# Kernel optimization log

Hardware: AMD Instinct MI355X
Metric: run time of the kernel (lower is better)

Reference implementation:

```python
import jax, jax.numpy as jnp
import numpy as np

N, M, E, D = 20000, 1024, 640000, 256


def setup_inputs() -> dict:
    key = jax.random.key(0)
    ks = jax.random.split(key, 24)
    mask = jax.random.uniform(ks[0], (N, M)) < 0.05
    init = jnp.where(mask, jax.random.uniform(ks[1], (N, M), minval=0.1, maxval=1.0), 0.0)
    inp = {
        'init': init,
        'ei_cc': jax.random.randint(ks[2], (2, E), 0, N, dtype=jnp.int32),
        'ei_cac': jax.random.randint(ks[3], (2, E), 0, N, dtype=jnp.int32),
        'ei_csc': jax.random.randint(ks[4], (2, E), 0, N, dtype=jnp.int32),
        'ea_cc': jax.random.uniform(ks[5], (E,), minval=0.1, maxval=1.0),
        'ea_cac': jax.random.uniform(ks[6], (E,), minval=0.1, maxval=1.0),
        'ea_csc': jax.random.uniform(ks[7], (E,), minval=0.1, maxval=1.0),
        # Projection MLP: Linear(1,16) -> ReLU -> Linear(16,D)
        'pW1': jax.random.normal(ks[8], (1, 16)) * 0.5,
        'pb1': jnp.zeros((16,)),
        'pW2': jax.random.normal(ks[9], (16, D)) * 0.1,
        'pb2': jnp.zeros((D,)),
        # three GCN branches, 3 layers each (all D->D)
        'W_cc': jax.random.normal(ks[10], (3, D, D)) * 0.05,
        'b_cc': jnp.zeros((3, D)),
        'W_cac': jax.random.normal(ks[11], (3, D, D)) * 0.05,
        'b_cac': jnp.zeros((3, D)),
        'W_csc': jax.random.normal(ks[12], (3, D, D)) * 0.05,
        'b_csc': jnp.zeros((3, D)),
        # meta-path attention: Linear(D, 1)
        'w_att': jax.random.normal(ks[13], (D,)) * 0.05,
        'b_att': jnp.zeros((1,)),
    }
    return inp


def projection(init, pW1, pb1, pW2, pb2):
    # torch code feeds the *indices* of nonzero columns through the MLP and
    # mean-pools per row. Vectorize: precompute MLP(j) for every column index j,
    # then masked mean.
    idx = jnp.arange(M, dtype=init.dtype)[:, None]          # [M, 1]
    h = jax.nn.relu(idx @ pW1 + pb1)                        # [M, 16]
    col_emb = h @ pW2 + pb2                                 # [M, D]
    mask = (init != 0).astype(init.dtype)                   # [N, M]
    cnt = mask.sum(axis=1)                                  # [N]
    emb = (mask @ col_emb) / jnp.maximum(cnt, 1.0)[:, None]
    return jnp.where(cnt[:, None] > 0, emb, 0.0)            # zero rows stay zero


def gcn_conv(x, edge_index, edge_weight, W, b):
    # PyG GCNConv with edge_weight: add self loops (w=1), symmetric norm.
    n = x.shape[0]
    loop = jnp.arange(n, dtype=edge_index.dtype)
    row = jnp.concatenate([edge_index[0], loop])
    col = jnp.concatenate([edge_index[1], loop])
    w = jnp.concatenate([edge_weight, jnp.ones((n,), x.dtype)])
    deg = jax.ops.segment_sum(w, col, num_segments=n)
    dinv = jnp.where(deg > 0, jax.lax.rsqrt(deg), 0.0)
    norm = dinv[row] * w * dinv[col]                        # [E+N]
    h = x @ W                                               # [N, D]
    out = jax.ops.segment_sum(norm[:, None] * h[row], col, num_segments=n)
    return out + b


def gcn_branch(x, edge_index, edge_weight, Ws, bs):
    for l in range(3):
        x = jax.nn.relu(gcn_conv(x, edge_index, edge_weight, Ws[l], bs[l]))
    return x


def reference(init, ei_cc, ei_cac, ei_csc, ea_cc, ea_cac, ea_csc,
              pW1, pb1, pW2, pb2, W_cc, b_cc, W_cac, b_cac, W_csc, b_csc,
              w_att, b_att):
    x0 = projection(init, pW1, pb1, pW2, pb2)               # [N, D]
    out_cc = gcn_branch(x0, ei_cc, ea_cc, W_cc, b_cc)
    out_cac = gcn_branch(x0, ei_cac, ea_cac, W_cac, b_cac)
    out_csc = gcn_branch(x0, ei_csc, ea_csc, W_csc, b_csc)
    emb = jnp.stack([out_cc, out_cac, out_csc], axis=0)     # [3, N, D]
    scores = jnp.einsum('pnd,d->pn', emb, w_att) + b_att[0] # [3, N]
    attn = jax.nn.softmax(scores, axis=0)                   # softmax over meta-paths
    return jnp.einsum('pn,pnd->nd', attn, emb)              # [N, D]
```

## Files before the change

kernel.cpp:

```cpp
#include <hip/hip_runtime.h>
#include <hip/hip_bf16.h>

typedef __hip_bfloat16 bf16;
typedef __bf16 v8bf __attribute__((ext_vector_type(8)));
typedef float f32x4 __attribute__((ext_vector_type(4)));
typedef unsigned int v4u __attribute__((ext_vector_type(4)));

constexpr int N = 20000, M = 1024, E = 640000, D = 256;
constexpr size_t SEGEL = (size_t)N * D;
constexpr int NCHUNK = 10000;
constexpr int NSLICE = 64;
constexpr int ESLICE = E / NSLICE;

__device__ __forceinline__ float b2f(bf16 v) { return __bfloat162float(v); }
__device__ __forceinline__ bf16 f2b(float f) { return __float2bfloat16(f); }
__device__ __forceinline__ float u2f(unsigned short u) { return __uint_as_float(((unsigned)u) << 16); }
__device__ __forceinline__ unsigned short f2u(float f) { bf16 h = __float2bfloat16(f); return *(unsigned short*)&h; }
__device__ __forceinline__ float loadf(const void* p, size_t i, int isbf) {
    return isbf ? b2f(((const bf16*)p)[i]) : ((const float*)p)[i];
}
__device__ __forceinline__ void fma8(float* acc, uint4 v, float w) {
    acc[0] = fmaf(w, u2f((unsigned short)(v.x & 0xffffu)), acc[0]);
    acc[1] = fmaf(w, u2f((unsigned short)(v.x >> 16)), acc[1]);
    acc[2] = fmaf(w, u2f((unsigned short)(v.y & 0xffffu)), acc[2]);
    acc[3] = fmaf(w, u2f((unsigned short)(v.y >> 16)), acc[3]);
    acc[4] = fmaf(w, u2f((unsigned short)(v.z & 0xffffu)), acc[4]);
    acc[5] = fmaf(w, u2f((unsigned short)(v.z >> 16)), acc[5]);
    acc[6] = fmaf(w, u2f((unsigned short)(v.w & 0xffffu)), acc[6]);
    acc[7] = fmaf(w, u2f((unsigned short)(v.w >> 16)), acc[7]);
}
__device__ __forceinline__ void add4(float* acc, uint2 v) {
    acc[0] += u2f((unsigned short)(v.x & 0xffffu));
    acc[1] += u2f((unsigned short)(v.x >> 16));
    acc[2] += u2f((unsigned short)(v.y & 0xffffu));
    acc[3] += u2f((unsigned short)(v.y >> 16));
}
__device__ __forceinline__ unsigned pack2(float a, float b) {
    return (unsigned)f2u(a) | ((unsigned)f2u(b) << 16);
}

__global__ void detect_kernel(const void* __restrict__ ea, int* __restrict__ flag)
{
    if (threadIdx.x == 0 && blockIdx.x == 0) {
        const unsigned short* u = (const unsigned short*)ea;
        int cnt = 0;
        for (int i = 0; i < 64; i++) {
            float f = __uint_as_float(((unsigned)u[i]) << 16);
            if (f >= 0.05f && f <= 1.05f) cnt++;
        }
        *flag = (cnt >= 60) ? 1 : 0;
    }
}

__global__ __launch_bounds__(256) void prep_kernel(
    const void* __restrict__ W0, const void* __restrict__ W1, const void* __restrict__ W2,
    const void* __restrict__ pW1, const void* __restrict__ pb1,
    const void* __restrict__ pW2, const void* __restrict__ pb2,
    bf16* __restrict__ WT, bf16* __restrict__ cemb, const int* __restrict__ flag)
{
    int isbf = *flag;
    int b = blockIdx.x;
    if (b < 2304) {
        int mat = b >> 8, n = b & 255, k = threadIdx.x;
        const void* W = (mat < 3) ? W0 : (mat < 6) ? W1 : W2;
        int lm = mat - (mat < 3 ? 0 : (mat < 6 ? 3 : 6));
        WT[(size_t)mat * 65536 + n * 256 + k] =
            f2b(loadf(W, (size_t)lm * 65536 + k * 256 + n, isbf));
    } else {
        int j = b - 2304;
        int d = threadIdx.x;
        float jf = (float)j;
        float acc = loadf(pb2, d, isbf);
        #pragma unroll
        for (int k = 0; k < 16; k++) {
            float h = fmaxf(jf * loadf(pW1, k, isbf) + loadf(pb1, k, isbf), 0.0f);
            acc += h * loadf(pW2, k * 256 + d, isbf);
        }
        cemb[(size_t)j * 256 + d] = f2b(acc);
    }
}

__global__ __launch_bounds__(256) void projection_kernel(
    const void* __restrict__ init, const bf16* __restrict__ cemb,
    bf16* __restrict__ x0, const int* __restrict__ flag)
{
    __shared__ unsigned short idxs[4][1024];
    int isbf = *flag;
    int wave = threadIdx.x >> 6, lane = threadIdx.x & 63;
    int i = blockIdx.x * 4 + wave;
    unsigned long long below = (lane == 63) ? 0x7fffffffffffffffull
                                            : ((1ull << lane) - 1ull);
    int cnt = 0;
    if (isbf) {
        const unsigned short* row = (const unsigned short*)init + (size_t)i * 1024;
        for (int c0 = 0; c0 < 1024; c0 += 64) {
            bool nz = (row[c0 + lane] & 0x7fffu) != 0;
            unsigned long long m = __ballot(nz);
            if (nz) idxs[wave][cnt + __popcll(m & below)] = (unsigned short)(c0 + lane);
            cnt += __popcll(m);
        }
    } else {
        const float* row = (const float*)init + (size_t)i * 1024;
        for (int c0 = 0; c0 < 1024; c0 += 64) {
            bool nz = row[c0 + lane] != 0.0f;
            unsigned long long m = __ballot(nz);
            if (nz) idxs[wave][cnt + __popcll(m & below)] = (unsigned short)(c0 + lane);
            cnt += __popcll(m);
        }
    }
    const uint2* cr = (const uint2*)cemb;
    float acc[4] = {0.0f, 0.0f, 0.0f, 0.0f};
    int j = 0;
    for (; j + 8 <= cnt; j += 8) {
        uint2 v0 = cr[(size_t)idxs[wave][j + 0] * 64 + lane];
        uint2 v1 = cr[(size_t)idxs[wave][j + 1] * 64 + lane];
        uint2 v2 = cr[(size_t)idxs[wave][j + 2] * 64 + lane];
        uint2 v3 = cr[(size_t)idxs[wave][j + 3] * 64 + lane];
        uint2 v4 = cr[(size_t)idxs[wave][j + 4] * 64 + lane];
        uint2 v5 = cr[(size_t)idxs[wave][j + 5] * 64 + lane];
        uint2 v6 = cr[(size_t)idxs[wave][j + 6] * 64 + lane];
        uint2 v7 = cr[(size_t)idxs[wave][j + 7] * 64 + lane];
        add4(acc, v0); add4(acc, v1); add4(acc, v2); add4(acc, v3);
        add4(acc, v4); add4(acc, v5); add4(acc, v6); add4(acc, v7);
    }
    for (; j < cnt; j++) {
        uint2 v = cr[(size_t)idxs[wave][j] * 64 + lane];
        add4(acc, v);
    }
    float rinv = 1.0f / fmaxf((float)cnt, 1.0f);
    uint2 o;
    o.x = pack2(acc[0] * rinv, acc[1] * rinv);
    o.y = pack2(acc[2] * rinv, acc[3] * rinv);
    ((uint2*)x0)[(size_t)i * 64 + lane] = o;
}

__global__ __launch_bounds__(256) void countP_kernel(
    const int* __restrict__ e0, const int* __restrict__ e1, const int* __restrict__ e2,
    int* __restrict__ P)
{
    __shared__ int cur[NCHUNK];
    int b = blockIdx.x;
    int pb = b >> 7, rem = b & 127;
    int ck = rem >> 6, s = rem & 63;
    const int* ei = pb == 0 ? e0 : pb == 1 ? e1 : e2;
    int c0 = ck * NCHUNK;
    int t = threadIdx.x;
    for (int i = t; i < NCHUNK; i += 256) cur[i] = 0;
    __syncthreads();
    int ebase = s * ESLICE;
    for (int e = ebase + t; e < ebase + ESLICE; e += 256) {
        int c = ei[E + e];
        if (c >= c0 && c < c0 + NCHUNK) atomicAdd(&cur[c - c0], 1);
    }
    __syncthreads();
    int* Prow = P + ((size_t)(pb * NSLICE + s)) * N + c0;
    for (int i = t; i < NCHUNK; i += 256) Prow[i] = cur[i];
}

__global__ __launch_bounds__(256) void cnt_sum_kernel(
    const int* __restrict__ P, int* __restrict__ cnt)
{
    int id = blockIdx.x * 256 + threadIdx.x;
    if (id >= 3 * N) return;
    int pb = id / N, c = id - pb * N;
    int sum = 0;
    #pragma unroll 8
    for (int s = 0; s < NSLICE; s++)
        sum += P[((size_t)(pb * NSLICE + s)) * N + c];
    cnt[id] = sum;
}

__global__ __launch_bounds__(1024) void scan_kernel(
    const int* __restrict__ cnt, int* __restrict__ col_ptr)
{
    int pb = blockIdx.x;
    int base = pb * E;
    __shared__ int s[1024];
    int t = threadIdx.x;
    const int CH = 20;
    int i0 = t * CH;
    int sum = 0;
    for (int j = 0; j < CH; j++) { int i = i0 + j; if (i < N) sum += cnt[pb * N + i]; }
    s[t] = sum;
    __syncthreads();
    for (int off = 1; off < 1024; off <<= 1) {
        int v = (t >= off) ? s[t - off] : 0;
        __syncthreads();
        s[t] += v;
        __syncthreads();
    }
    int run = base + s[t] - sum;
    for (int j = 0; j < CH; j++) {
        int i = i0 + j;
        if (i < N) {
            col_ptr[pb * (N + 1) + i] = run;
            run += cnt[pb * N + i];
        }
    }
    if (t == 0) col_ptr[pb * (N + 1) + N] = base + E;
}

__global__ __launch_bounds__(256) void base_kernel(
    int* __restrict__ P, const int* __restrict__ col_ptr)
{
    int id = blockIdx.x * 256 + threadIdx.x;
    if (id >= 3 * N) return;
    int pb = id / N, c = id - pb * N;
    int run = col_ptr[pb * (N + 1) + c];
    for (int s = 0; s < NSLICE; s++) {
        size_t idx = ((size_t)(pb * NSLICE + s)) * N + c;
        int v = P[idx];
        P[idx] = run;
        run += v;
    }
}

__global__ __launch_bounds__(256) void fill_kernel(
    const int* __restrict__ e0, const int* __restrict__ e1, const int* __restrict__ e2,
    const void* __restrict__ a0, const void* __restrict__ a1, const void* __restrict__ a2,
    const int* __restrict__ P, int2* __restrict__ epack, const int* __restrict__ flag)
{
    __shared__ int cur[NCHUNK];
    int isbf = *flag;
    int b = blockIdx.x;
    int pb = b >> 7, rem = b & 127;
    int ck = rem >> 6, s = rem & 63;
    const int* ei = pb == 0 ? e0 : pb == 1 ? e1 : e2;
    const void* ea = pb == 0 ? a0 : pb == 1 ? a1 : a2;
    int c0 = ck * NCHUNK;
    int t = threadIdx.x;
    const int* Prow = P + ((size_t)(pb * NSLICE + s)) * N + c0;
    for (int i = t; i < NCHUNK; i += 256) cur[i] = Prow[i];
    __syncthreads();
    int ebase = s * ESLICE;
    for (int e = ebase + t; e < ebase + ESLICE; e += 256) {
        int c = ei[E + e];
        if (c >= c0 && c < c0 + NCHUNK) {
            int r = ei[e];
            float w = loadf(ea, e, isbf);
            int pos = atomicAdd(&cur[c - c0], 1);
            int2 v; v.x = r; v.y = __float_as_int(w);
            epack[pos] = v;
        }
    }
}

__global__ __launch_bounds__(256) void degsum_kernel(
    const int* __restrict__ col_ptr, const int2* __restrict__ epack,
    float* __restrict__ dinv, float* __restrict__ nloop)
{
    int wave = threadIdx.x >> 6, lane = threadIdx.x & 63;
    int pb = blockIdx.x / 5000;
    int i = (blockIdx.x - pb * 5000) * 4 + wave;
    int start = col_ptr[pb * (N + 1) + i], end = col_ptr[pb * (N + 1) + i + 1];
    float sum = 0.0f;
    for (int p = start + lane; p < end; p += 64) sum += __int_as_float(epack[p].y);
    for (int off = 1; off < 64; off <<= 1) sum += __shfl_xor(sum, off, 64);
    if (lane == 0) {
        float dg = 1.0f + sum;
        dinv[pb * N + i] = rsqrtf(dg);
        nloop[pb * N + i] = 1.0f / dg;
    }
}

__global__ __launch_bounds__(256) void snorm_sort_kernel(
    const int* __restrict__ col_ptr, int2* __restrict__ epack,
    const float* __restrict__ dinv)
{
    int wave = threadIdx.x >> 6, lane = threadIdx.x & 63;
    int pb = blockIdx.x / 5000;
    int i = (blockIdx.x - pb * 5000) * 4 + wave;
    int start = col_ptr[pb * (N + 1) + i], end = col_ptr[pb * (N + 1) + i + 1];
    float dc = dinv[pb * N + i];
    for (int base = start; base < end; base += 64) {
        int n = end - base; n = n < 64 ? n : 64;
        int key = 0x7fffffff, val = 0;
        if (lane < n) {
            int2 v = epack[base + lane];
            key = v.x;
            val = __float_as_int(dc * __int_as_float(v.y) * dinv[pb * N + v.x]);
        }
        #pragma unroll
        for (int k = 2; k <= 64; k <<= 1) {
            #pragma unroll
            for (int j = k >> 1; j > 0; j >>= 1) {
                int pk = __shfl_xor(key, j, 64);
                int pv = __shfl_xor(val, j, 64);
                bool up = (lane & k) == 0;
                bool lower = (lane & j) == 0;
                bool takeMin = (up == lower);
                bool sw = takeMin ? (pk < key) : (pk > key);
                if (sw) { key = pk; val = pv; }
            }
        }
        if (lane < n) {
            int2 o; o.x = key; o.y = val;
            epack[base + lane] = o;
        }
    }
}

__global__ __launch_bounds__(256) void aggregate_kernel(
    const bf16* __restrict__ xi0, const bf16* __restrict__ xi1, const bf16* __restrict__ xi2,
    bf16* __restrict__ yb,
    const int* __restrict__ col_ptr, const int2* __restrict__ epack,
    const float* __restrict__ nloop)
{
    int wave = threadIdx.x >> 6, lane = threadIdx.x & 63;
    int pb = blockIdx.x / 5000;
    int i = (blockIdx.x - pb * 5000) * 4 + wave;
    const bf16* x = pb == 0 ? xi0 : pb == 1 ? xi1 : xi2;
    const uint4* xr = (const uint4*)x;
    int L = lane & 31, h = lane >> 5;
    int start = col_ptr[pb * (N + 1) + i], end = col_ptr[pb * (N + 1) + i + 1];
    float nl = nloop[pb * N + i];
    float acc[8];
    {
        uint4 sv = xr[(size_t)i * 32 + L];
        float self = (h == 0) ? nl : 0.0f;
        #pragma unroll
        for (int j = 0; j < 8; j++) acc[j] = 0.0f;
        fma8(acc, sv, self);
    }
    for (int base = start; base < end; base += 64) {
        int n = end - base; n = n < 64 ? n : 64;
        int ex = 0, ey = 0;
        if (lane < n) {
            unsigned long long ev = __builtin_nontemporal_load(
                (const unsigned long long*)(epack + base + lane));
            ex = (int)(unsigned)(ev & 0xffffffffull);
            ey = (int)(unsigned)(ev >> 32);
        }
        int pmax = (n + 1) >> 1;
        int p0 = 0;
        for (; p0 + 8 <= pmax; p0 += 8) {
            int eb = 2 * p0 + h;
            int r0 = __shfl(ex, eb +  0, 64);
            int r1 = __shfl(ex, eb +  2, 64);
            int r2 = __shfl(ex, eb +  4, 64);
            int r3 = __shfl(ex, eb +  6, 64);
            int r4 = __shfl(ex, eb +  8, 64);
            int r5 = __shfl(ex, eb + 10, 64);
            int r6 = __shfl(ex, eb + 12, 64);
            int r7 = __shfl(ex, eb + 14, 64);
            float w0 = __int_as_float(__shfl(ey, eb +  0, 64));
            float w1 = __int_as_float(__shfl(ey, eb +  2, 64));
            float w2 = __int_as_float(__shfl(ey, eb +  4, 64));
            float w3 = __int_as_float(__shfl(ey, eb +  6, 64));
            float w4 = __int_as_float(__shfl(ey, eb +  8, 64));
            float w5 = __int_as_float(__shfl(ey, eb + 10, 64));
            float w6 = __int_as_float(__shfl(ey, eb + 12, 64));
            float w7 = __int_as_float(__shfl(ey, eb + 14, 64));
            uint4 v0 = xr[(size_t)r0 * 32 + L];
            uint4 v1 = xr[(size_t)r1 * 32 + L];
            uint4 v2 = xr[(size_t)r2 * 32 + L];
            uint4 v3 = xr[(size_t)r3 * 32 + L];
            uint4 v4 = xr[(size_t)r4 * 32 + L];
            uint4 v5 = xr[(size_t)r5 * 32 + L];
            uint4 v6 = xr[(size_t)r6 * 32 + L];
            uint4 v7 = xr[(size_t)r7 * 32 + L];
            fma8(acc, v0, w0); fma8(acc, v1, w1);
            fma8(acc, v2, w2); fma8(acc, v3, w3);
            fma8(acc, v4, w4); fma8(acc, v5, w5);
            fma8(acc, v6, w6); fma8(acc, v7, w7);
        }
        if (p0 + 4 <= pmax) {
            int eb = 2 * p0 + h;
            int r0 = __shfl(ex, eb + 0, 64);
            int r1 = __shfl(ex, eb + 2, 64);
            int r2 = __shfl(ex, eb + 4, 64);
            int r3 = __shfl(ex, eb + 6, 64);
            float w0 = __int_as_float(__shfl(ey, eb + 0, 64));
            float w1 = __int_as_float(__shfl(ey, eb + 2, 64));
            float w2 = __int_as_float(__shfl(ey, eb + 4, 64));
            float w3 = __int_as_float(__shfl(ey, eb + 6, 64));
            uint4 v0 = xr[(size_t)r0 * 32 + L];
            uint4 v1 = xr[(size_t)r1 * 32 + L];
            uint4 v2 = xr[(size_t)r2 * 32 + L];
            uint4 v3 = xr[(size_t)r3 * 32 + L];
            fma8(acc, v0, w0); fma8(acc, v1, w1);
            fma8(acc, v2, w2); fma8(acc, v3, w3);
            p0 += 4;
        }
        for (; p0 < pmax; p0++) {
            int e = 2 * p0 + h;
            int rj = __shfl(ex, e, 64);
            float w = __int_as_float(__shfl(ey, e, 64));
            uint4 v = xr[(size_t)rj * 32 + L];
            fma8(acc, v, w);
        }
    }
    #pragma unroll
    for (int j = 0; j < 8; j++) acc[j] += __shfl_xor(acc[j], 32, 64);
    if (h == 0) {
        v4u o;
        o.x = pack2(acc[0], acc[1]);
        o.y = pack2(acc[2], acc[3]);
        o.z = pack2(acc[4], acc[5]);
        o.w = pack2(acc[6], acc[7]);
        __builtin_nontemporal_store(o,
            (v4u*)yb + (size_t)pb * (SEGEL / 8) + (size_t)i * 32 + L);
    }
}

__global__ __launch_bounds__(256) void gemm_relu_kernel(
    const bf16* __restrict__ yb, const bf16* __restrict__ WT, int layer,
    const void* __restrict__ b0, const void* __restrict__ b1, const void* __restrict__ b2,
    bf16* __restrict__ o0, bf16* __restrict__ o1, bf16* __restrict__ o2,
    const int* __restrict__ flag)
{
    int isbf = *flag;
    int pl = blockIdx.x / 625, blk = blockIdx.x - pl * 625;
    const bf16* y = yb + (size_t)pl * SEGEL;
    const bf16* wt = WT + (size_t)(pl * 3 + layer) * 65536;
    const void* bias = pl == 0 ? b0 : pl == 1 ? b1 : b2;
    bf16* xout = pl == 0 ? o0 : pl == 1 ? o1 : o2;

    int wave = threadIdx.x >> 6, lane = threadIdx.x & 63;
    int m0 = blk * 32 + (wave >> 1) * 16;
    int n0 = (wave & 1) * 128;
    int mrow = lane & 15, q = lane >> 4;

    f32x4 acc[8] = {};
    const v8bf* arow = reinterpret_cast<const v8bf*>(y + (size_t)(m0 + mrow) * 256);
    for (int k0 = 0; k0 < 256; k0 += 32) {
        v8bf a = arow[(k0 >> 3) + q];
        #pragma unroll
        for (int nt = 0; nt < 8; nt++) {
            const v8bf* brow = reinterpret_cast<const v8bf*>(wt + (size_t)(n0 + nt * 16 + mrow) * 256);
            acc[nt] = __builtin_amdgcn_mfma_f32_16x16x32_bf16(a, brow[(k0 >> 3) + q], acc[nt], 0, 0, 0);
        }
    }
    #pragma unroll
    for (int nt = 0; nt < 8; nt++) {
        int col = n0 + nt * 16 + mrow;
        float bv = loadf(bias, (size_t)layer * 256 + col, isbf);
        #pragma unroll
        for (int r = 0; r < 4; r++) {
            int row = m0 + q * 4 + r;
            xout[(size_t)row * 256 + col] = f2b(fmaxf(acc[nt][r] + bv, 0.0f));
        }
    }
}

__global__ __launch_bounds__(256) void attention_kernel(
    const bf16* __restrict__ e0, const bf16* __restrict__ e1, const bf16* __restrict__ e2,
    const void* __restrict__ w_att, void* __restrict__ out, int n_nodes,
    const int* __restrict__ flag)
{
    int isbf = *flag;
    int wave = threadIdx.x >> 6, lane = threadIdx.x & 63;
    int n = blockIdx.x * 4 + wave;
    if (n >= n_nodes) return;
    int d0 = lane * 4;
    float w[4], v0[4], v1[4], v2[4];
    #pragma unroll
    for (int j = 0; j < 4; j++) {
        w[j]  = loadf(w_att, d0 + j, isbf);
        v0[j] = b2f(e0[(size_t)n * 256 + d0 + j]);
        v1[j] = b2f(e1[(size_t)n * 256 + d0 + j]);
        v2[j] = b2f(e2[(size_t)n * 256 + d0 + j]);
    }
    float s0 = 0, s1 = 0, s2 = 0;
    #pragma unroll
    for (int j = 0; j < 4; j++) { s0 += v0[j] * w[j]; s1 += v1[j] * w[j]; s2 += v2[j] * w[j]; }
    for (int off = 1; off < 64; off <<= 1) {
        s0 += __shfl_xor(s0, off, 64);
        s1 += __shfl_xor(s1, off, 64);
        s2 += __shfl_xor(s2, off, 64);
    }
    float m = fmaxf(s0, fmaxf(s1, s2));
    float a0 = expf(s0 - m), a1 = expf(s1 - m), a2 = expf(s2 - m);
    float inv = 1.0f / (a0 + a1 + a2);
    a0 *= inv; a1 *= inv; a2 *= inv;
    #pragma unroll
    for (int j = 0; j < 4; j++) {
        float v = a0 * v0[j] + a1 * v1[j] + a2 * v2[j];
        if (isbf) ((bf16*)out)[(size_t)n * 256 + d0 + j] = f2b(v);
        else      ((float*)out)[(size_t)n * 256 + d0 + j] = v;
    }
}

extern "C" void kernel_launch(void* const* d_in, const int* in_sizes, int n_in,
                              void* d_out, int out_size, void* d_ws, size_t ws_size,
                              hipStream_t stream)
{
    (void)in_sizes; (void)n_in; (void)out_size; (void)ws_size;

    const void* init = d_in[0];
    const int*  ei[3] = {(const int*)d_in[1], (const int*)d_in[2], (const int*)d_in[3]};
    const void* ea[3] = {d_in[4], d_in[5], d_in[6]};
    const void* pW1 = d_in[7];
    const void* pb1 = d_in[8];
    const void* pW2 = d_in[9];
    const void* pb2 = d_in[10];
    const void* Wb[3] = {d_in[11], d_in[13], d_in[15]};
    const void* bb[3] = {d_in[12], d_in[14], d_in[16]};
    const void* w_att = d_in[17];

    char* ws = (char*)d_ws;
    size_t off = 0;
    auto carve = [&](size_t bytes) -> char* {
        off = (off + 255) & ~(size_t)255;
        char* p = ws + off; off += bytes; return p;
    };
    int*   flag  = (int*)carve(4);
    bf16*  WT    = (bf16*)carve((size_t)9 * 65536 * 2);
    bf16*  cemb  = (bf16*)carve((size_t)M * D * 2);
    bf16*  x0    = (bf16*)carve(SEGEL * 2);
    int*   cnt   = (int*)carve((size_t)3 * N * 4);
    int*   colp  = (int*)carve((size_t)3 * (N + 1) * 4);
    float* dinv  = (float*)carve((size_t)3 * N * 4);
    float* nloop = (float*)carve((size_t)3 * N * 4);
    int2*  epack = (int2*)carve((size_t)3 * E * 8);
    bf16*  ybuf  = (bf16*)carve((size_t)3 * SEGEL * 2);
    bf16*  bufA  = (bf16*)carve((size_t)3 * SEGEL * 2);
    bf16*  bufB  = (bf16*)carve((size_t)3 * SEGEL * 2);
    int* P = (int*)bufB;

    detect_kernel<<<1, 64, 0, stream>>>(ea[0], flag);
    prep_kernel<<<3328, 256, 0, stream>>>(Wb[0], Wb[1], Wb[2],
                                          pW1, pb1, pW2, pb2, WT, cemb, flag);
    projection_kernel<<<5000, 256, 0, stream>>>(init, cemb, x0, flag);

    countP_kernel<<<384, 256, 0, stream>>>(ei[0], ei[1], ei[2], P);
    cnt_sum_kernel<<<(3 * N + 255) / 256, 256, 0, stream>>>(P, cnt);
    scan_kernel<<<3, 1024, 0, stream>>>(cnt, colp);
    base_kernel<<<(3 * N + 255) / 256, 256, 0, stream>>>(P, colp);
    fill_kernel<<<384, 256, 0, stream>>>(ei[0], ei[1], ei[2], ea[0], ea[1], ea[2],
                                         P, epack, flag);
    degsum_kernel<<<15000, 256, 0, stream>>>(colp, epack, dinv, nloop);
    snorm_sort_kernel<<<15000, 256, 0, stream>>>(colp, epack, dinv);

    const bf16 *i0 = x0, *i1 = x0, *i2 = x0;
    bf16* dsts[3] = {bufA, bufB, bufA};
    for (int l = 0; l < 3; l++) {
        aggregate_kernel<<<15000, 256, 0, stream>>>(i0, i1, i2, ybuf, colp, epack, nloop);
        bf16* dst = dsts[l];
        gemm_relu_kernel<<<1875, 256, 0, stream>>>(ybuf, WT, l, bb[0], bb[1], bb[2],
                                                   dst, dst + SEGEL, dst + 2 * SEGEL, flag);
        i0 = dst; i1 = dst + SEGEL; i2 = dst + 2 * SEGEL;
    }
    attention_kernel<<<5000, 256, 0, stream>>>(bufA, bufA + SEGEL, bufA + 2 * SEGEL,
                                               w_att, d_out, N, flag);
}
```

Baseline: 907.9 us.

## Fuse final GEMM with meta-path attention and remap aggregate blocks by XCD

The last layer's GEMM+ReLU is fused with the attention softmax. Each block computes all three branches for 32 rows, keeps the bf16-rounded results in registers, reduces the scores through shared memory, and writes the blended output directly. This removes the write and re-read of the three final embedding buffers and one kernel launch. Separately, aggregate blocks are remapped so each XCD (block index mod 8) works on a single branch, which should improve L2 locality for the gathered rows; the grid grows to 20000 blocks, some of which exit immediately. The fused kernel holds many registers and runs only 625 blocks, so occupancy may be low.

```diff
diff --git a/kernel.cpp b/kernel.cpp
--- a/kernel.cpp
+++ b/kernel.cpp
@@ -306,9 +306,15 @@
     const int* __restrict__ col_ptr, const int2* __restrict__ epack,
     const float* __restrict__ nloop)
 {
+    int b = blockIdx.x;
+    int xcd = b & 7, rnd = b >> 3;
+    int pb, seq;
+    if (xcd < 3)      { pb = 0; seq = rnd * 3 + xcd; }
+    else if (xcd < 6) { pb = 1; seq = rnd * 3 + (xcd - 3); }
+    else              { pb = 2; seq = rnd * 2 + (xcd - 6); }
+    if (seq >= 5000) return;
     int wave = threadIdx.x >> 6, lane = threadIdx.x & 63;
-    int pb = blockIdx.x / 5000;
-    int i = (blockIdx.x - pb * 5000) * 4 + wave;
+    int i = seq * 4 + wave;
     const bf16* x = pb == 0 ? xi0 : pb == 1 ? xi1 : xi2;
     const uint4* xr = (const uint4*)x;
     int L = lane & 31, h = lane >> 5;
@@ -443,41 +449,89 @@
     }
 }
 
-__global__ __launch_bounds__(256) void attention_kernel(
-    const bf16* __restrict__ e0, const bf16* __restrict__ e1, const bf16* __restrict__ e2,
-    const void* __restrict__ w_att, void* __restrict__ out, int n_nodes,
+__global__ __launch_bounds__(256) void gemm_attn_kernel(
+    const bf16* __restrict__ yb, const bf16* __restrict__ WT,
+    const void* __restrict__ b0, const void* __restrict__ b1, const void* __restrict__ b2,
+    const void* __restrict__ w_att, void* __restrict__ out,
     const int* __restrict__ flag)
 {
+    __shared__ float sc[3][32];
     int isbf = *flag;
+    int blk = blockIdx.x;
     int wave = threadIdx.x >> 6, lane = threadIdx.x & 63;
-    int n = blockIdx.x * 4 + wave;
-    if (n >= n_nodes) return;
-    int d0 = lane * 4;
-    float w[4], v0[4], v1[4], v2[4];
+    int wm = wave >> 1;
+    int m0 = blk * 32 + wm * 16;
+    int n0 = (wave & 1) * 128;
+    int mrow = lane & 15, q = lane >> 4;
+
+    if (threadIdx.x < 96) ((float*)sc)[threadIdx.x] = 0.0f;
+    __syncthreads();
+
+    unsigned pe[3][8][2];
     #pragma unroll
-    for (int j = 0; j < 4; j++) {
-        w[j]  = loadf(w_att, d0 + j, isbf);
-        v0[j] = b2f(e0[(size_t)n * 256 + d0 + j]);
-        v1[j] = b2f(e1[(size_t)n * 256 + d0 + j]);
-        v2[j] = b2f(e2[(size_t)n * 256 + d0 + j]);
-    }
-    float s0 = 0, s1 = 0, s2 = 0;
+    for (int p = 0; p < 3; p++) {
+        const bf16* y = yb + (size_t)p * SEGEL;
+        const bf16* wt = WT + (size_t)(p * 3 + 2) * 65536;
+        const void* bias = p == 0 ? b0 : p == 1 ? b1 : b2;
+        f32x4 acc[8] = {};
+        const v8bf* arow = reinterpret_cast<const v8bf*>(y + (size_t)(m0 + mrow) * 256);
+        for (int k0 = 0; k0 < 256; k0 += 32) {
+            v8bf a = arow[(k0 >> 3) + q];
+            #pragma unroll
+            for (int nt = 0; nt < 8; nt++) {
+                const v8bf* brow = reinterpret_cast<const v8bf*>(wt + (size_t)(n0 + nt * 16 + mrow) * 256);
+                acc[nt] = __builtin_amdgcn_mfma_f32_16x16x32_bf16(a, brow[(k0 >> 3) + q], acc[nt], 0, 0, 0);
+            }
+        }
+        float part[4] = {0.0f, 0.0f, 0.0f, 0.0f};
+        #pragma unroll
+        for (int nt = 0; nt < 8; nt++) {
+            int col = n0 + nt * 16 + mrow;
+            float bv = loadf(bias, (size_t)2 * 256 + col, isbf);
+            float wv = loadf(w_att, col, isbf);
+            float e0 = u2f(f2u(fmaxf(acc[nt][0] + bv, 0.0f)));
+            float e1 = u2f(f2u(fmaxf(acc[nt][1] + bv, 0.0f)));
+            float e2 = u2f(f2u(fmaxf(acc[nt][2] + bv, 0.0f)));
+            float e3 = u2f(f2u(fmaxf(acc[nt][3] + bv, 0.0f)));
+            pe[p][nt][0] = pack2(e0, e1);
+            pe[p][nt][1] = pack2(e2, e3);
+            part[0] = fmaf(e0, wv, part[0]);
+            part[1] = fmaf(e1, wv, part[1]);
+            part[2] = fmaf(e2, wv, part[2]);
+            part[3] = fmaf(e3, wv, part[3]);
+        }
+        #pragma unroll
+        for (int off = 1; off < 16; off <<= 1) {
+            #pragma unroll
+            for (int r = 0; r < 4; r++) part[r] += __shfl_xor(part[r], off, 64);
+        }
+        if (mrow == 0) {
+            #pragma unroll
+            for (int r = 0; r < 4; r++)
+                atomicAdd(&sc[p][wm * 16 + q * 4 + r], part[r]);
+        }
+    }
+    __syncthreads();
     #pragma unroll
-    for (int j = 0; j < 4; j++) { s0 += v0[j] * w[j]; s1 += v1[j] * w[j]; s2 += v2[j] * w[j]; }
-    for (int off = 1; off < 64; off <<= 1) {
-        s0 += __shfl_xor(s0, off, 64);
-        s1 += __shfl_xor(s1, off, 64);
-        s2 += __shfl_xor(s2, off, 64);
-    }
-    float m = fmaxf(s0, fmaxf(s1, s2));
-    float a0 = expf(s0 - m), a1 = expf(s1 - m), a2 = expf(s2 - m);
-    float inv = 1.0f / (a0 + a1 + a2);
-    a0 *= inv; a1 *= inv; a2 *= inv;
-    #pragma unroll
-    for (int j = 0; j < 4; j++) {
-        float v = a0 * v0[j] + a1 * v1[j] + a2 * v2[j];
-        if (isbf) ((bf16*)out)[(size_t)n * 256 + d0 + j] = f2b(v);
-        else      ((float*)out)[(size_t)n * 256 + d0 + j] = v;
+    for (int r = 0; r < 4; r++) {
+        int lrow = wm * 16 + q * 4 + r;
+        float s0 = sc[0][lrow], s1 = sc[1][lrow], s2 = sc[2][lrow];
+        float mx = fmaxf(s0, fmaxf(s1, s2));
+        float a0 = expf(s0 - mx), a1 = expf(s1 - mx), a2 = expf(s2 - mx);
+        float inv = 1.0f / (a0 + a1 + a2);
+        a0 *= inv; a1 *= inv; a2 *= inv;
+        int row = blk * 32 + lrow;
+        #pragma unroll
+        for (int nt = 0; nt < 8; nt++) {
+            int col = n0 + nt * 16 + mrow;
+            unsigned w0 = pe[0][nt][r >> 1], w1 = pe[1][nt][r >> 1], w2 = pe[2][nt][r >> 1];
+            float v0 = u2f((unsigned short)((r & 1) ? (w0 >> 16) : (w0 & 0xffffu)));
+            float v1 = u2f((unsigned short)((r & 1) ? (w1 >> 16) : (w1 & 0xffffu)));
+            float v2 = u2f((unsigned short)((r & 1) ? (w2 >> 16) : (w2 & 0xffffu)));
+            float v = a0 * v0 + a1 * v1 + a2 * v2;
+            if (isbf) ((bf16*)out)[(size_t)row * 256 + col] = f2b(v);
+            else      ((float*)out)[(size_t)row * 256 + col] = v;
+        }
     }
 }
 
@@ -533,14 +587,16 @@
     snorm_sort_kernel<<<15000, 256, 0, stream>>>(colp, epack, dinv);
 
     const bf16 *i0 = x0, *i1 = x0, *i2 = x0;
-    bf16* dsts[3] = {bufA, bufB, bufA};
     for (int l = 0; l < 3; l++) {
-        aggregate_kernel<<<15000, 256, 0, stream>>>(i0, i1, i2, ybuf, colp, epack, nloop);
-        bf16* dst = dsts[l];
-        gemm_relu_kernel<<<1875, 256, 0, stream>>>(ybuf, WT, l, bb[0], bb[1], bb[2],
-                                                   dst, dst + SEGEL, dst + 2 * SEGEL, flag);
-        i0 = dst; i1 = dst + SEGEL; i2 = dst + 2 * SEGEL;
-    }
-    attention_kernel<<<5000, 256, 0, stream>>>(bufA, bufA + SEGEL, bufA + 2 * SEGEL,
-                                               w_att, d_out, N, flag);
-}
+        aggregate_kernel<<<20000, 256, 0, stream>>>(i0, i1, i2, ybuf, colp, epack, nloop);
+        if (l < 2) {
+            bf16* dst = (l == 0) ? bufA : bufB;
+            gemm_relu_kernel<<<1875, 256, 0, stream>>>(ybuf, WT, l, bb[0], bb[1], bb[2],
+                                                       dst, dst + SEGEL, dst + 2 * SEGEL, flag);
+            i0 = dst; i1 = dst + SEGEL; i2 = dst + 2 * SEGEL;
+        } else {
+            gemm_attn_kernel<<<625, 256, 0, stream>>>(ybuf, WT, bb[0], bb[1], bb[2],
+                                                      w_att, d_out, flag);
+        }
+    }
+}
```

After: 967.6 us. +6.6%, slower.
